# Kernel tuning notes

Hardware: AMD Instinct MI355X
Metric: run time of the kernel (lower is better)

Reference implementation:

```python
import jax, jax.numpy as jnp
import numpy as np

DIM = 512  # word_hidden_size * 2


def _linear_params(key, din, dout, scale=0.05):
    kw, kb = jax.random.split(key)
    W = jax.random.normal(kw, (din, dout), dtype=jnp.float32) * scale
    b = jax.random.normal(kb, (dout,), dtype=jnp.float32) * scale
    return W, b


def setup_inputs() -> dict:
    key = jax.random.key(0)
    ks = jax.random.split(key, 16)
    S_c, S_q, B = 256, 32, 32
    inp = {
        'context_output': jax.random.normal(ks[0], (S_c, B, DIM), dtype=jnp.float32),
        'question_output': jax.random.normal(ks[1], (S_q, B, DIM), dtype=jnp.float32),
        'question_hidden_state': jax.random.normal(ks[2], (B, DIM), dtype=jnp.float32),
        'image_output': jax.random.normal(ks[3], (S_c, B, DIM), dtype=jnp.float32),
    }
    names = ['fc1', 'fc2', 'dm', 'rm', 'qm', 'rr', 'rg', 'qg']
    for i, n in enumerate(names):
        W, b = _linear_params(ks[4 + i], DIM, DIM)
        inp['W_' + n] = W
        inp['b_' + n] = b
    W_ms, b_ms = _linear_params(ks[12], DIM, 1)
    inp['W_ms'] = W_ms
    inp['b_ms'] = b_ms
    return inp


def reference(context_output, question_output, question_hidden_state, image_output,
              W_fc1, b_fc1, W_fc2, b_fc2, W_dm, b_dm, W_rm, b_rm, W_qm, b_qm,
              W_rr, b_rr, W_rg, b_rg, W_qg, b_qg, W_ms, b_ms):
    # ctx: [B, S, D] = fc1(context) + fc2(image) after seq-first -> batch-first permute
    ctx = (jnp.einsum('sbd,de->bse', context_output, W_fc1) + b_fc1
           + jnp.einsum('sbd,de->bse', image_output, W_fc2) + b_fc2)
    # hoist loop-invariant linear_dm(ctx): same math, computed once
    ctx_dm = jnp.einsum('bsd,de->bse', ctx, W_dm) + b_dm  # [B, S, D]

    B = ctx.shape[0]
    r0 = jnp.zeros((B, DIM), dtype=ctx.dtype)

    def step(r, q_t):  # r: [B, D], q_t: [B, D]
        rm = r @ W_rm + b_rm          # [B, D]
        qm = q_t @ W_qm + b_qm        # [B, D]
        m = jnp.tanh(ctx_dm + rm[:, None, :] + qm[:, None, :])  # [B, S, D]
        logits = jnp.einsum('bsd,do->bso', m, W_ms)[..., 0] + b_ms[0]  # [B, S]
        s = jax.nn.softmax(logits, axis=1)                     # [B, S]
        r_new = jnp.einsum('bs,bsd->bd', s, ctx) + jnp.tanh(r @ W_rr + b_rr)
        return r_new, None

    r, _ = jax.lax.scan(step, r0, question_output)  # scan over question tokens

    g = (r @ W_rg + b_rg) + (question_hidden_state @ W_qg + b_qg)  # [B, D]
    return g
```

## Files before the change

### kernel.cpp

```cpp
#include <hip/hip_runtime.h>
#include <hip/hip_bf16.h>

#define DIMD 512
#define NB   32
#define NS   256
#define NT   32
#define SA_STR  66
#define SCT_STR 258
#define SR_STR  132

typedef __bf16 bf16x8 __attribute__((ext_vector_type(8)));
typedef float  f32x4  __attribute__((ext_vector_type(4)));

__device__ __forceinline__ float tanh_fast(float x) {
    float e = __expf(2.f * x);
    return 1.f - 2.f / (e + 1.f);
}

__device__ __forceinline__ void gl_lds16(const __bf16* g, __bf16* l) {
    __builtin_amdgcn_global_load_lds((const __attribute__((address_space(1))) void*)g,
                                     (__attribute__((address_space(3))) void*)l, 16, 0, 0);
}


__global__ void k_prep(const float* __restrict__ ctxin, const float* __restrict__ img,
                       const float* __restrict__ qin,
                       __bf16* __restrict__ acat, __bf16* __restrict__ qp) {
    int row = blockIdx.x;
    if (row < 8192) {
        int b = row >> 8, s = row & 255;
        const float* c  = ctxin + ((size_t)s * NB + b) * DIMD;
        const float* im = img   + ((size_t)s * NB + b) * DIMD;
        __bf16* o = acat + (size_t)row * 1024;
        for (int d = threadIdx.x; d < DIMD; d += 256) {
            o[d]       = (__bf16)c[d];
            o[512 + d] = (__bf16)im[d];
        }
    } else {
        int idx = (row - 8192) * 256 + threadIdx.x;
        qp[idx] = (__bf16)qin[idx];
    }
}

__global__ void k_transpose_w6(const float* __restrict__ s0, const float* __restrict__ s1,
                               const float* __restrict__ s2, const float* __restrict__ s3,
                               const float* __restrict__ s4_, const float* __restrict__ s5,
                               __bf16* __restrict__ d01, __bf16* __restrict__ d2,
                               __bf16* __restrict__ d3, __bf16* __restrict__ d4,
                               __bf16* __restrict__ d5) {
    __shared__ float tile[32][33];
    int z = blockIdx.z;
    const float* src = (z == 0) ? s0 : (z == 1) ? s1 : (z == 2) ? s2
                     : (z == 3) ? s3 : (z == 4) ? s4_ : s5;
    __bf16* dst; int stride, off;
    if (z < 2) { dst = d01; stride = 1024; off = z * 512; }
    else {
        dst = (z == 2) ? d2 : (z == 3) ? d3 : (z == 4) ? d4 : d5;
        stride = 512; off = 0;
    }
    int c0 = blockIdx.x * 32, r0 = blockIdx.y * 32;
    int x = threadIdx.x, y = threadIdx.y;
#pragma unroll
    for (int k = 0; k < 32; k += 8)
        tile[y + k][x] = src[(size_t)(r0 + y + k) * DIMD + c0 + x];
    __syncthreads();
#pragma unroll
    for (int k = 0; k < 32; k += 8)
        dst[(size_t)(c0 + y + k) * stride + off + r0 + x] = (__bf16)tile[x][y + k];
}

__global__ void k_post_t(const __bf16* __restrict__ ctxb, __bf16* __restrict__ ctxT,
                         const float* __restrict__ Wrg, const float* __restrict__ Wqg,
                         __bf16* __restrict__ wrgT, __bf16* __restrict__ wqgT) {
    int z = blockIdx.z;
    int x = threadIdx.x, y = threadIdx.y;
    if (z < 32) {
        if (blockIdx.y >= 8) return;
        __shared__ __bf16 tile[32][33];
        int c0 = blockIdx.x * 32, s0 = blockIdx.y * 32;
        const __bf16* S = ctxb + (size_t)z * NS * DIMD;
        __bf16* D = ctxT + (size_t)z * DIMD * NS;
#pragma unroll
        for (int k = 0; k < 32; k += 8)
            tile[y + k][x] = S[(size_t)(s0 + y + k) * DIMD + c0 + x];
        __syncthreads();
#pragma unroll
        for (int k = 0; k < 32; k += 8)
            D[(size_t)(c0 + y + k) * NS + s0 + x] = tile[x][y + k];
    } else {
        __shared__ float tf[32][33];
        const float* src = (z == 32) ? Wrg : Wqg;
        __bf16* dst = (z == 32) ? wrgT : wqgT;
        int c0 = blockIdx.x * 32, r0 = blockIdx.y * 32;
#pragma unroll
        for (int k = 0; k < 32; k += 8)
            tf[y + k][x] = src[(size_t)(r0 + y + k) * DIMD + c0 + x];
        __syncthreads();
#pragma unroll
        for (int k = 0; k < 32; k += 8)
            dst[(size_t)(c0 + y + k) * DIMD + r0 + x] = (__bf16)tf[x][y + k];
    }
}

__global__ void k_gemm64(const __bf16* __restrict__ A, const __bf16* __restrict__ BT,
                         const float* __restrict__ bias1, const float* __restrict__ bias2,
                         void* __restrict__ out, int M, int N, int K, int out_f32) {
    __shared__ __bf16 As[64 * 64];
    __shared__ __bf16 Bs[64 * 64];
    int tid = threadIdx.x, wave = tid >> 6, lane = tid & 63;
    int wm = wave >> 1, wn = wave & 1;
    int m0 = blockIdx.x * 64, n0 = blockIdx.y * 64;
    int lr = lane & 15, lq = lane >> 4;

    f32x4 acc[2][2];
#pragma unroll
    for (int i = 0; i < 2; i++)
#pragma unroll
        for (int j = 0; j < 2; j++) acc[i][j] = (f32x4){0.f, 0.f, 0.f, 0.f};

    int g0 = (wave * 2 + 0) * 64 + lane;
    int g1 = (wave * 2 + 1) * 64 + lane;
    int r0_ = g0 >> 3, c0_ = g0 & 7;
    int r1_ = g1 >> 3, c1_ = g1 & 7;
    __bf16* la0 = As + (wave * 2 + 0) * 512;
    __bf16* la1 = As + (wave * 2 + 1) * 512;
    __bf16* lb0 = Bs + (wave * 2 + 0) * 512;
    __bf16* lb1 = Bs + (wave * 2 + 1) * 512;

    for (int kk = 0; kk < K; kk += 64) {
        gl_lds16(A  + (size_t)(m0 + r0_) * K + kk + c0_ * 8, la0);
        gl_lds16(A  + (size_t)(m0 + r1_) * K + kk + c1_ * 8, la1);
        gl_lds16(BT + (size_t)(n0 + r0_) * K + kk + c0_ * 8, lb0);
        gl_lds16(BT + (size_t)(n0 + r1_) * K + kk + c1_ * 8, lb1);
        __syncthreads();
#pragma unroll
        for (int k2 = 0; k2 < 64; k2 += 32) {
            bf16x8 af[2], bfv[2];
#pragma unroll
            for (int i = 0; i < 2; i++)
                af[i] = *(const bf16x8*)(As + (wm * 32 + i * 16 + lr) * 64 + k2 + lq * 8);
#pragma unroll
            for (int j = 0; j < 2; j++)
                bfv[j] = *(const bf16x8*)(Bs + (wn * 32 + j * 16 + lr) * 64 + k2 + lq * 8);
#pragma unroll
            for (int i = 0; i < 2; i++)
#pragma unroll
                for (int j = 0; j < 2; j++)
                    acc[i][j] = __builtin_amdgcn_mfma_f32_16x16x32_bf16(af[i], bfv[j], acc[i][j], 0, 0, 0);
        }
        __syncthreads();
    }

#pragma unroll
    for (int i = 0; i < 2; i++)
#pragma unroll
        for (int j = 0; j < 2; j++) {
            int col = n0 + wn * 32 + j * 16 + lr;
            float bs = bias1[col] + (bias2 ? bias2[col] : 0.f);
#pragma unroll
            for (int r = 0; r < 4; r++) {
                int row = m0 + wm * 32 + i * 16 + lq * 4 + r;
                float v = acc[i][j][r] + bs;
                if (out_f32) ((float*)out)[(size_t)row * N + col] = v;
                else         ((__bf16*)out)[(size_t)row * N + col] = (__bf16)v;
            }
        }
}


__device__ __forceinline__ void bflag(unsigned* fb, int j, unsigned tgt) {
    __syncthreads();
    if (threadIdx.x == 0) {
        __atomic_signal_fence(__ATOMIC_SEQ_CST);
        __builtin_amdgcn_s_waitcnt(0x0F70);
        __atomic_signal_fence(__ATOMIC_SEQ_CST);
        __hip_atomic_store(fb + j * 16, tgt, __ATOMIC_RELAXED, __HIP_MEMORY_SCOPE_AGENT);
    }
    if (threadIdx.x < 8) {
        while (__hip_atomic_load(fb + threadIdx.x * 16, __ATOMIC_RELAXED,
                                 __HIP_MEMORY_SCOPE_AGENT) < tgt)
            __builtin_amdgcn_s_sleep(1);
    }
    __syncthreads();
}

__global__ __launch_bounds__(512, 2) void k_scan(
    const __bf16* __restrict__ ctxdm,
    const __bf16* __restrict__ ctxT,
    const __bf16* __restrict__ wrmT,
    const __bf16* __restrict__ wrrT,
    const float* __restrict__ qmf,
    const float* __restrict__ wms, const float* __restrict__ brm,
    const float* __restrict__ brr,
    float* partials,
    float* rpub,
    unsigned* flags,
    float* __restrict__ rbuf) {
    int bid = blockIdx.x;
    int b = bid >> 3, j = bid & 7;
    int tid = threadIdx.x, wave = tid >> 6, lane = tid & 63;
    int g = lane >> 3, i = lane & 7;

    __shared__ __bf16 sA[256 * SA_STR];
    __shared__ __bf16 sCT[64 * SCT_STR];
    __shared__ float  sQ[NT * 64];
    __shared__ float  spart[NS];
    __shared__ float  sp[NS];
    __shared__ float  sq[512];
    __shared__ float  s4[4];
    __shared__ float  sps[8 * 68];
    __shared__ float  srm[64], sh[64];
    __shared__ float  sr4[4 * SR_STR];
    __shared__ float  smv[512];

    unsigned* fb = flags + b * 8 * 16;

    for (int c = tid; c < 2048; c += 512) {
        int row = c >> 3, c8 = c & 7;
        *(bf16x8*)(sA + row * SA_STR + c8 * 8) =
            *(const bf16x8*)(ctxdm + ((size_t)(b * NS + row)) * DIMD + j * 64 + c8 * 8);
    }
    for (int c = tid; c < 2048; c += 512) {
        int col = c >> 5, s8 = c & 31;
        *(bf16x8*)(sCT + col * SCT_STR + s8 * 8) =
            *(const bf16x8*)(ctxT + ((size_t)(b * DIMD) + j * 64 + col) * NS + s8 * 8);
    }
    for (int c = tid; c < NT * 64; c += 512) {
        int tt = c >> 6, e = c & 63;
        sQ[c] = qmf[((size_t)tt * NB + b) * DIMD + j * 64 + e];
    }
    int m = tid >> 8, cl = (tid >> 2) & 63, q = tid & 3;
    const __bf16* wp = (m ? wrrT : wrmT) + ((size_t)(j * 64 + cl)) * DIMD + q * 128;
    bf16x8 wreg[16];
#pragma unroll
    for (int u = 0; u < 16; u++) wreg[u] = *(const bf16x8*)(wp + u * 8);

    float wm[8];
#pragma unroll
    for (int u = 0; u < 8; u++) wm[u] = wms[j * 64 + i * 8 + u];
    if (tid < 64) {
        srm[tid] = brm[j * 64 + tid];
        sh[tid]  = tanh_fast(brr[j * 64 + tid]);
    }
    __syncthreads();

    unsigned ph = 1;
    for (int t = 0; t < NT; t++) {
        float rq[8];
#pragma unroll
        for (int u = 0; u < 8; u++) rq[u] = srm[i * 8 + u] + sQ[t * 64 + i * 8 + u];
#pragma unroll
        for (int k = 0; k < 4; k++) {
            int s = wave * 32 + k * 8 + g;
            bf16x8 cv = *(const bf16x8*)(sA + s * SA_STR + i * 8);
            float a = 0.f;
#pragma unroll
            for (int u = 0; u < 8; u++)
                a += tanh_fast((float)cv[u] + rq[u]) * wm[u];
            a += __shfl_xor(a, 1); a += __shfl_xor(a, 2); a += __shfl_xor(a, 4);
            if (i == 0) spart[s] = a;
        }
        __syncthreads();
        if (tid < NS)
            __hip_atomic_store(&partials[(b * 8 + j) * NS + tid], spart[tid],
                               __ATOMIC_RELAXED, __HIP_MEMORY_SCOPE_AGENT);
        bflag(fb, j, ph); ph++;

        {
            int s = tid >> 1, jh = (tid & 1) * 4;
            float a = 0.f;
#pragma unroll
            for (int u = 0; u < 4; u++)
                a += __hip_atomic_load(&partials[(b * 8 + jh + u) * NS + s],
                                       __ATOMIC_RELAXED, __HIP_MEMORY_SCOPE_AGENT);
            sq[tid] = a;
        }
        __syncthreads();
        float ev = 0.f;
        if (tid < NS) { ev = __expf(sq[2 * tid] + sq[2 * tid + 1]); sp[tid] = ev; }
#pragma unroll
        for (int off = 32; off; off >>= 1) ev += __shfl_xor(ev, off);
        if (tid < NS && lane == 0) s4[wave] = ev;
        __syncthreads();
        float inv = 1.f / (s4[0] + s4[1] + s4[2] + s4[3]);
        {
            const __bf16* cp = sCT + lane * SCT_STR + wave * 32;
            const float* pp = sp + wave * 32;
            float a = 0.f;
#pragma unroll
            for (int k = 0; k < 32; k += 8) {
                bf16x8 v = *(const bf16x8*)(cp + k);
#pragma unroll
                for (int u = 0; u < 8; u++) a = fmaf(pp[k + u], (float)v[u], a);
            }
            sps[wave * 68 + lane] = a;
        }
        __syncthreads();
        if (tid < 64) {
            float a = 0.f;
#pragma unroll
            for (int w2 = 0; w2 < 8; w2++) a += sps[w2 * 68 + tid];
            float rv = a * inv + sh[tid];
            if (t == NT - 1) rbuf[b * DIMD + j * 64 + tid] = rv;
            else
                __hip_atomic_store(&rpub[b * DIMD + j * 64 + tid], rv,
                                   __ATOMIC_RELAXED, __HIP_MEMORY_SCOPE_AGENT);
        }
        if (t == NT - 1) break;
        bflag(fb, j, ph); ph++;

        sr4[(tid >> 7) * SR_STR + (tid & 127)] =
            __hip_atomic_load(&rpub[b * DIMD + tid], __ATOMIC_RELAXED, __HIP_MEMORY_SCOPE_AGENT);
        __syncthreads();
        {
            const float* sv = sr4 + q * SR_STR;
            float a0 = 0.f, a1 = 0.f;
#pragma unroll
            for (int u = 0; u < 16; u += 2) {
                bf16x8 w0 = wreg[u], w1 = wreg[u + 1];
#pragma unroll
                for (int e = 0; e < 8; e++) {
                    a0 = fmaf(sv[u * 8 + e],     (float)w0[e], a0);
                    a1 = fmaf(sv[u * 8 + 8 + e], (float)w1[e], a1);
                }
            }
            smv[tid] = a0 + a1;
        }
        __syncthreads();
        if (tid < 128) {
            int m2 = tid >> 6, cl3 = tid & 63;
            float a = smv[m2 * 256 + cl3 * 4] + smv[m2 * 256 + cl3 * 4 + 1]
                    + smv[m2 * 256 + cl3 * 4 + 2] + smv[m2 * 256 + cl3 * 4 + 3];
            int col = j * 64 + cl3;
            if (m2 == 0) srm[cl3] = a + brm[col];
            else         sh[cl3]  = tanh_fast(a + brr[col]);
        }
        __syncthreads();
    }
}

__global__ void k_final2(const float* __restrict__ r, const float* __restrict__ qh,
                         const __bf16* __restrict__ wrgT, const __bf16* __restrict__ wqgT,
                         const float* __restrict__ brg, const float* __restrict__ bqg,
                         float* __restrict__ out) {
    int clx = threadIdx.x & 7, b = threadIdx.x >> 3;
    int col = blockIdx.x * 8 + clx;
    const __bf16* w1 = wrgT + (size_t)col * DIMD;
    const __bf16* w2 = wqgT + (size_t)col * DIMD;
    const float* rp = r + (size_t)b * DIMD;
    const float* qp = qh + (size_t)b * DIMD;
    float acc = brg[col] + bqg[col];
#pragma unroll 4
    for (int d = 0; d < DIMD; d += 8) {
        bf16x8 a = *(const bf16x8*)(w1 + d);
        bf16x8 c = *(const bf16x8*)(w2 + d);
#pragma unroll
        for (int u = 0; u < 8; u++)
            acc += rp[d + u] * (float)a[u] + qp[d + u] * (float)c[u];
    }
    out[b * DIMD + col] = acc;
}


extern "C" void kernel_launch(void* const* d_in, const int* in_sizes, int n_in,
                              void* d_out, int out_size, void* d_ws, size_t ws_size,
                              hipStream_t stream) {
    const float* ctx_in = (const float*)d_in[0];
    const float* q_in   = (const float*)d_in[1];
    const float* qh     = (const float*)d_in[2];
    const float* img    = (const float*)d_in[3];
    const float* W_fc1  = (const float*)d_in[4];
    const float* b_fc1  = (const float*)d_in[5];
    const float* W_fc2  = (const float*)d_in[6];
    const float* b_fc2  = (const float*)d_in[7];
    const float* W_dm   = (const float*)d_in[8];
    const float* b_dm   = (const float*)d_in[9];
    const float* W_rm   = (const float*)d_in[10];
    const float* b_rm   = (const float*)d_in[11];
    const float* W_qm   = (const float*)d_in[12];
    const float* b_qm   = (const float*)d_in[13];
    const float* W_rr   = (const float*)d_in[14];
    const float* b_rr   = (const float*)d_in[15];
    const float* W_rg   = (const float*)d_in[16];
    const float* b_rg   = (const float*)d_in[17];
    const float* W_qg   = (const float*)d_in[18];
    const float* b_qg   = (const float*)d_in[19];
    const float* W_ms   = (const float*)d_in[20];

    char* w = (char*)d_ws;
    __bf16* acat  = (__bf16*)w;  w += (size_t)8192 * 1024 * 2;
    __bf16* qp    = (__bf16*)w;  w += (size_t)1024 * 512 * 2;
    __bf16* wcatT = (__bf16*)w;  w += (size_t)512 * 1024 * 2;
    __bf16* wdmT  = (__bf16*)w;  w += (size_t)512 * 512 * 2;
    __bf16* wqmT  = (__bf16*)w;  w += (size_t)512 * 512 * 2;
    __bf16* wrmT2 = (__bf16*)w;  w += (size_t)512 * 512 * 2;
    __bf16* wrrT2 = (__bf16*)w;  w += (size_t)512 * 512 * 2;
    __bf16* ctxb  = (__bf16*)w;  w += (size_t)8192 * 512 * 2;
    __bf16* ctxdm = (__bf16*)w;  w += (size_t)8192 * 512 * 2;
    char* x = (char*)acat;
    __bf16*   ctxT  = (__bf16*)x;    x += (size_t)NB * DIMD * NS * 2;
    float*    qmf   = (float*)x;     x += (size_t)1024 * 512 * 4;
    __bf16*   wrgT  = (__bf16*)x;    x += (size_t)512 * 512 * 2;
    __bf16*   wqgT  = (__bf16*)x;    x += (size_t)512 * 512 * 2;
    float*    rpub  = (float*)x;     x += (size_t)NB * DIMD * 4;
    float*    parts = (float*)x;     x += (size_t)NB * 8 * NS * 4;
    float*    rbuf  = (float*)x;     x += (size_t)NB * DIMD * 4;
    unsigned* flags = (unsigned*)x;  x += (size_t)256 * 16 * 4;

    k_prep<<<10240, 256, 0, stream>>>(ctx_in, img, q_in, acat, qp);
    k_transpose_w6<<<dim3(16, 16, 6), dim3(32, 8), 0, stream>>>(
        W_fc1, W_fc2, W_dm, W_qm, W_rm, W_rr, wcatT, wdmT, wqmT, wrmT2, wrrT2);

    k_gemm64<<<dim3(128, 8), 256, 0, stream>>>(acat, wcatT, b_fc1, b_fc2, ctxb, 8192, 512, 1024, 0);
    k_post_t<<<dim3(16, 16, 34), dim3(32, 8), 0, stream>>>(ctxb, ctxT, W_rg, W_qg, wrgT, wqgT);
    k_gemm64<<<dim3(128, 8), 256, 0, stream>>>(ctxb, wdmT, b_dm, nullptr, ctxdm, 8192, 512, 512, 0);
    k_gemm64<<<dim3(16, 8), 256, 0, stream>>>(qp, wqmT, b_qm, nullptr, qmf, 1024, 512, 512, 1);

    hipMemsetAsync(flags, 0, (size_t)256 * 16 * 4, stream);

    k_scan<<<256, 512, 0, stream>>>(ctxdm, ctxT, wrmT2, wrrT2, qmf, W_ms,
                                    b_rm, b_rr, parts, rpub, flags, rbuf);

    k_final2<<<64, 256, 0, stream>>>(rbuf, qh, wrgT, wqgT, b_rg, b_qg, (float*)d_out);
}
```

Measured before the change: 501.3 us.

## Fold fc and dm projections into one wide GEMM with precomputed combined weights

Precomputes the product of the concatenated fc1/fc2 weights with W_dm, plus a matching folded bias, so ctx and ctx_dm come out of a single 8192x1024x1024 GEMM reading the concatenated input. This replaces the two dependent GEMMs, removing the serial dependency on the intermediate ctx and one kernel launch. The scan kernel now reads ctx_dm from the upper half of the combined buffer, and its block-to-(batch, slice) mapping is also reordered. The cost is a small extra weight GEMM, and ctx_dm picks up slightly different bf16 rounding because it is computed from the raw inputs rather than from rounded ctx.

```diff
diff --git a/kernel.cpp b/kernel.cpp
--- a/kernel.cpp
+++ b/kernel.cpp
@@ -24,8 +24,10 @@
 
 
 __global__ void k_prep(const float* __restrict__ ctxin, const float* __restrict__ img,
-                       const float* __restrict__ qin,
-                       __bf16* __restrict__ acat, __bf16* __restrict__ qp) {
+                       const float* __restrict__ qin, const float* __restrict__ Wfc1,
+                       const float* __restrict__ Wfc2,
+                       __bf16* __restrict__ acat, __bf16* __restrict__ qp,
+                       __bf16* __restrict__ wcat_nt) {
     int row = blockIdx.x;
     if (row < 8192) {
         int b = row >> 8, s = row & 255;
@@ -36,9 +38,12 @@
             o[d]       = (__bf16)c[d];
             o[512 + d] = (__bf16)im[d];
         }
-    } else {
+    } else if (row < 10240) {
         int idx = (row - 8192) * 256 + threadIdx.x;
         qp[idx] = (__bf16)qin[idx];
+    } else {
+        int idx = (row - 10240) * 256 + threadIdx.x;
+        wcat_nt[idx] = (__bf16)(idx < 262144 ? Wfc1[idx] : Wfc2[idx - 262144]);
     }
 }
 
@@ -69,7 +74,19 @@
         dst[(size_t)(c0 + y + k) * stride + off + r0 + x] = (__bf16)tile[x][y + k];
 }
 
-__global__ void k_post_t(const __bf16* __restrict__ ctxb, __bf16* __restrict__ ctxT,
+__global__ void k_bias(const float* __restrict__ bfc1, const float* __restrict__ bfc2,
+                       const float* __restrict__ Wdm, const float* __restrict__ bdm,
+                       float* __restrict__ bias_big) {
+    int o = blockIdx.x * 256 + threadIdx.x;
+    if (o < 512) { bias_big[o] = bfc1[o] + bfc2[o]; return; }
+    int od = o - 512;
+    float acc = bdm[od];
+    for (int d = 0; d < 512; d++)
+        acc += (bfc1[d] + bfc2[d]) * Wdm[(size_t)d * 512 + od];
+    bias_big[o] = acc;
+}
+
+__global__ void k_post_t(const __bf16* __restrict__ ctxbig, __bf16* __restrict__ ctxT,
                          const float* __restrict__ Wrg, const float* __restrict__ Wqg,
                          __bf16* __restrict__ wrgT, __bf16* __restrict__ wqgT) {
     int z = blockIdx.z;
@@ -78,11 +95,11 @@
         if (blockIdx.y >= 8) return;
         __shared__ __bf16 tile[32][33];
         int c0 = blockIdx.x * 32, s0 = blockIdx.y * 32;
-        const __bf16* S = ctxb + (size_t)z * NS * DIMD;
+        const __bf16* S = ctxbig + (size_t)z * NS * 1024;
         __bf16* D = ctxT + (size_t)z * DIMD * NS;
 #pragma unroll
         for (int k = 0; k < 32; k += 8)
-            tile[y + k][x] = S[(size_t)(s0 + y + k) * DIMD + c0 + x];
+            tile[y + k][x] = S[(size_t)(s0 + y + k) * 1024 + c0 + x];
         __syncthreads();
 #pragma unroll
         for (int k = 0; k < 32; k += 8)
@@ -156,7 +173,7 @@
 #pragma unroll
         for (int j = 0; j < 2; j++) {
             int col = n0 + wn * 32 + j * 16 + lr;
-            float bs = bias1[col] + (bias2 ? bias2[col] : 0.f);
+            float bs = (bias1 ? bias1[col] : 0.f) + (bias2 ? bias2[col] : 0.f);
 #pragma unroll
             for (int r = 0; r < 4; r++) {
                 int row = m0 + wm * 32 + i * 16 + lq * 4 + r;
@@ -185,7 +202,7 @@
 }
 
 __global__ __launch_bounds__(512, 2) void k_scan(
-    const __bf16* __restrict__ ctxdm,
+    const __bf16* __restrict__ ctxbig,
     const __bf16* __restrict__ ctxT,
     const __bf16* __restrict__ wrmT,
     const __bf16* __restrict__ wrrT,
@@ -197,7 +214,7 @@
     unsigned* flags,
     float* __restrict__ rbuf) {
     int bid = blockIdx.x;
-    int b = bid >> 3, j = bid & 7;
+    int b = bid & 31, j = bid >> 5;
     int tid = threadIdx.x, wave = tid >> 6, lane = tid & 63;
     int g = lane >> 3, i = lane & 7;
 
@@ -218,7 +235,7 @@
     for (int c = tid; c < 2048; c += 512) {
         int row = c >> 3, c8 = c & 7;
         *(bf16x8*)(sA + row * SA_STR + c8 * 8) =
-            *(const bf16x8*)(ctxdm + ((size_t)(b * NS + row)) * DIMD + j * 64 + c8 * 8);
+            *(const bf16x8*)(ctxbig + ((size_t)(b * NS + row)) * 1024 + 512 + j * 64 + c8 * 8);
     }
     for (int c = tid; c < 2048; c += 512) {
         int col = c >> 5, s8 = c & 31;
@@ -388,15 +405,16 @@
     const float* W_ms   = (const float*)d_in[20];
 
     char* w = (char*)d_ws;
-    __bf16* acat  = (__bf16*)w;  w += (size_t)8192 * 1024 * 2;
-    __bf16* qp    = (__bf16*)w;  w += (size_t)1024 * 512 * 2;
-    __bf16* wcatT = (__bf16*)w;  w += (size_t)512 * 1024 * 2;
-    __bf16* wdmT  = (__bf16*)w;  w += (size_t)512 * 512 * 2;
-    __bf16* wqmT  = (__bf16*)w;  w += (size_t)512 * 512 * 2;
-    __bf16* wrmT2 = (__bf16*)w;  w += (size_t)512 * 512 * 2;
-    __bf16* wrrT2 = (__bf16*)w;  w += (size_t)512 * 512 * 2;
-    __bf16* ctxb  = (__bf16*)w;  w += (size_t)8192 * 512 * 2;
-    __bf16* ctxdm = (__bf16*)w;  w += (size_t)8192 * 512 * 2;
+    __bf16* acat   = (__bf16*)w;  w += (size_t)8192 * 1024 * 2;
+    __bf16* qp     = (__bf16*)w;  w += (size_t)1024 * 512 * 2;
+    __bf16* btc    = (__bf16*)w;  w += (size_t)1024 * 1024 * 2;
+    __bf16* wdmT   = (__bf16*)w;  w += (size_t)512 * 512 * 2;
+    __bf16* wqmT   = (__bf16*)w;  w += (size_t)512 * 512 * 2;
+    __bf16* wrmT2  = (__bf16*)w;  w += (size_t)512 * 512 * 2;
+    __bf16* wrrT2  = (__bf16*)w;  w += (size_t)512 * 512 * 2;
+    float*  biasb  = (float*)w;   w += (size_t)1024 * 4;
+    __bf16* ctxbig = (__bf16*)w;  w += (size_t)8192 * 1024 * 2;
+    __bf16* wcat_nt = ctxbig;
     char* x = (char*)acat;
     __bf16*   ctxT  = (__bf16*)x;    x += (size_t)NB * DIMD * NS * 2;
     float*    qmf   = (float*)x;     x += (size_t)1024 * 512 * 4;
@@ -407,18 +425,20 @@
     float*    rbuf  = (float*)x;     x += (size_t)NB * DIMD * 4;
     unsigned* flags = (unsigned*)x;  x += (size_t)256 * 16 * 4;
 
-    k_prep<<<10240, 256, 0, stream>>>(ctx_in, img, q_in, acat, qp);
+    k_prep<<<12288, 256, 0, stream>>>(ctx_in, img, q_in, W_fc1, W_fc2, acat, qp, wcat_nt);
     k_transpose_w6<<<dim3(16, 16, 6), dim3(32, 8), 0, stream>>>(
-        W_fc1, W_fc2, W_dm, W_qm, W_rm, W_rr, wcatT, wdmT, wqmT, wrmT2, wrrT2);
-
-    k_gemm64<<<dim3(128, 8), 256, 0, stream>>>(acat, wcatT, b_fc1, b_fc2, ctxb, 8192, 512, 1024, 0);
-    k_post_t<<<dim3(16, 16, 34), dim3(32, 8), 0, stream>>>(ctxb, ctxT, W_rg, W_qg, wrgT, wqgT);
-    k_gemm64<<<dim3(128, 8), 256, 0, stream>>>(ctxb, wdmT, b_dm, nullptr, ctxdm, 8192, 512, 512, 0);
+        W_fc1, W_fc2, W_dm, W_qm, W_rm, W_rr, btc, wdmT, wqmT, wrmT2, wrrT2);
+    k_bias<<<4, 256, 0, stream>>>(b_fc1, b_fc2, W_dm, b_dm, biasb);
+    k_gemm64<<<dim3(8, 16), 256, 0, stream>>>(wdmT, wcat_nt, nullptr, nullptr,
+                                              btc + (size_t)512 * 1024, 512, 1024, 512, 0);
+    k_gemm64<<<dim3(128, 16), 256, 0, stream>>>(acat, btc, biasb, nullptr,
+                                                ctxbig, 8192, 1024, 1024, 0);
+    k_post_t<<<dim3(16, 16, 34), dim3(32, 8), 0, stream>>>(ctxbig, ctxT, W_rg, W_qg, wrgT, wqgT);
     k_gemm64<<<dim3(16, 8), 256, 0, stream>>>(qp, wqmT, b_qm, nullptr, qmf, 1024, 512, 512, 1);
 
     hipMemsetAsync(flags, 0, (size_t)256 * 16 * 4, stream);
 
-    k_scan<<<256, 512, 0, stream>>>(ctxdm, ctxT, wrmT2, wrrT2, qmf, W_ms,
+    k_scan<<<256, 512, 0, stream>>>(ctxbig, ctxT, wrmT2, wrrT2, qmf, W_ms,
                                     b_rm, b_rr, parts, rpub, flags, rbuf);
 
     k_final2<<<64, 256, 0, stream>>>(rbuf, qh, wrgT, wqgT, b_rg, b_qg, (float*)d_out);
```

New measurement: 525.1 us. 1.05x slower.

## Replace flag barriers with tagged 64-bit publish/poll and fuse prep kernels

Applied to the files above, without the earlier changes.

The per-step flag barriers in the recurrent scan are replaced by packing each published float with a step tag in one 64-bit atomic word. Consumers spin on exactly the values they need instead of waiting on a group-wide flag barrier. This removes two barrier rounds per step and the flag memset. Block indexing is remapped so that the eight blocks sharing a batch row are spaced 32 apart. The input-cast and weight-transpose kernels are merged into one launch. The tradeoff is doubled traffic for the published data, and correctness depends on stale tags in reused workspace never matching the current step.

```diff
diff --git a/kernel.cpp b/kernel.cpp
--- a/kernel.cpp
+++ b/kernel.cpp
@@ -11,6 +11,7 @@
 
 typedef __bf16 bf16x8 __attribute__((ext_vector_type(8)));
 typedef float  f32x4  __attribute__((ext_vector_type(4)));
+typedef unsigned long long u64;
 
 __device__ __forceinline__ float tanh_fast(float x) {
     float e = __expf(2.f * x);
@@ -22,10 +23,28 @@
                                      (__attribute__((address_space(3))) void*)l, 16, 0, 0);
 }
 
-
-__global__ void k_prep(const float* __restrict__ ctxin, const float* __restrict__ img,
-                       const float* __restrict__ qin,
-                       __bf16* __restrict__ acat, __bf16* __restrict__ qp) {
+__device__ __forceinline__ void pub64(u64* p, float v, unsigned tag) {
+    u64 pk = ((u64)__float_as_uint(v) << 32) | (u64)tag;
+    __hip_atomic_store(p, pk, __ATOMIC_RELAXED, __HIP_MEMORY_SCOPE_AGENT);
+}
+__device__ __forceinline__ float poll64(const u64* p, unsigned tag) {
+    u64 v = __hip_atomic_load(p, __ATOMIC_RELAXED, __HIP_MEMORY_SCOPE_AGENT);
+    while ((unsigned)v != tag) {
+        __builtin_amdgcn_s_sleep(1);
+        v = __hip_atomic_load(p, __ATOMIC_RELAXED, __HIP_MEMORY_SCOPE_AGENT);
+    }
+    return __uint_as_float((unsigned)(v >> 32));
+}
+
+__global__ void k_prep_all(const float* __restrict__ ctxin, const float* __restrict__ img,
+                           const float* __restrict__ qin,
+                           const float* __restrict__ Wfc1, const float* __restrict__ Wfc2,
+                           const float* __restrict__ Wdm, const float* __restrict__ Wqm,
+                           const float* __restrict__ Wrm, const float* __restrict__ Wrr,
+                           __bf16* __restrict__ acat, __bf16* __restrict__ qp,
+                           __bf16* __restrict__ wcatT, __bf16* __restrict__ wdmT,
+                           __bf16* __restrict__ wqmT, __bf16* __restrict__ wrmT,
+                           __bf16* __restrict__ wrrT) {
     int row = blockIdx.x;
     if (row < 8192) {
         int b = row >> 8, s = row & 255;
@@ -36,37 +55,32 @@
             o[d]       = (__bf16)c[d];
             o[512 + d] = (__bf16)im[d];
         }
-    } else {
+    } else if (row < 10240) {
         int idx = (row - 8192) * 256 + threadIdx.x;
         qp[idx] = (__bf16)qin[idx];
-    }
-}
-
-__global__ void k_transpose_w6(const float* __restrict__ s0, const float* __restrict__ s1,
-                               const float* __restrict__ s2, const float* __restrict__ s3,
-                               const float* __restrict__ s4_, const float* __restrict__ s5,
-                               __bf16* __restrict__ d01, __bf16* __restrict__ d2,
-                               __bf16* __restrict__ d3, __bf16* __restrict__ d4,
-                               __bf16* __restrict__ d5) {
-    __shared__ float tile[32][33];
-    int z = blockIdx.z;
-    const float* src = (z == 0) ? s0 : (z == 1) ? s1 : (z == 2) ? s2
-                     : (z == 3) ? s3 : (z == 4) ? s4_ : s5;
-    __bf16* dst; int stride, off;
-    if (z < 2) { dst = d01; stride = 1024; off = z * 512; }
-    else {
-        dst = (z == 2) ? d2 : (z == 3) ? d3 : (z == 4) ? d4 : d5;
-        stride = 512; off = 0;
-    }
-    int c0 = blockIdx.x * 32, r0 = blockIdx.y * 32;
-    int x = threadIdx.x, y = threadIdx.y;
-#pragma unroll
-    for (int k = 0; k < 32; k += 8)
-        tile[y + k][x] = src[(size_t)(r0 + y + k) * DIMD + c0 + x];
-    __syncthreads();
-#pragma unroll
-    for (int k = 0; k < 32; k += 8)
-        dst[(size_t)(c0 + y + k) * stride + off + r0 + x] = (__bf16)tile[x][y + k];
+    } else {
+        __shared__ float tile[32][33];
+        int zz = (row - 10240) >> 8;
+        int idx = (row - 10240) & 255;
+        int bx = idx & 15, by = idx >> 4;
+        int x = threadIdx.x & 31, y = threadIdx.x >> 5;
+        const float* src = (zz == 0) ? Wfc1 : (zz == 1) ? Wfc2 : (zz == 2) ? Wdm
+                         : (zz == 3) ? Wqm : (zz == 4) ? Wrm : Wrr;
+        __bf16* dst; int stride, off;
+        if (zz < 2) { dst = wcatT; stride = 1024; off = zz * 512; }
+        else {
+            dst = (zz == 2) ? wdmT : (zz == 3) ? wqmT : (zz == 4) ? wrmT : wrrT;
+            stride = 512; off = 0;
+        }
+        int c0 = bx * 32, r0 = by * 32;
+#pragma unroll
+        for (int k = 0; k < 32; k += 8)
+            tile[y + k][x] = src[(size_t)(r0 + y + k) * DIMD + c0 + x];
+        __syncthreads();
+#pragma unroll
+        for (int k = 0; k < 32; k += 8)
+            dst[(size_t)(c0 + y + k) * stride + off + r0 + x] = (__bf16)tile[x][y + k];
+    }
 }
 
 __global__ void k_post_t(const __bf16* __restrict__ ctxb, __bf16* __restrict__ ctxT,
@@ -156,7 +170,7 @@
 #pragma unroll
         for (int j = 0; j < 2; j++) {
             int col = n0 + wn * 32 + j * 16 + lr;
-            float bs = bias1[col] + (bias2 ? bias2[col] : 0.f);
+            float bs = (bias1 ? bias1[col] : 0.f) + (bias2 ? bias2[col] : 0.f);
 #pragma unroll
             for (int r = 0; r < 4; r++) {
                 int row = m0 + wm * 32 + i * 16 + lq * 4 + r;
@@ -165,23 +179,6 @@
                 else         ((__bf16*)out)[(size_t)row * N + col] = (__bf16)v;
             }
         }
-}
-
-
-__device__ __forceinline__ void bflag(unsigned* fb, int j, unsigned tgt) {
-    __syncthreads();
-    if (threadIdx.x == 0) {
-        __atomic_signal_fence(__ATOMIC_SEQ_CST);
-        __builtin_amdgcn_s_waitcnt(0x0F70);
-        __atomic_signal_fence(__ATOMIC_SEQ_CST);
-        __hip_atomic_store(fb + j * 16, tgt, __ATOMIC_RELAXED, __HIP_MEMORY_SCOPE_AGENT);
-    }
-    if (threadIdx.x < 8) {
-        while (__hip_atomic_load(fb + threadIdx.x * 16, __ATOMIC_RELAXED,
-                                 __HIP_MEMORY_SCOPE_AGENT) < tgt)
-            __builtin_amdgcn_s_sleep(1);
-    }
-    __syncthreads();
 }
 
 __global__ __launch_bounds__(512, 2) void k_scan(
@@ -192,12 +189,11 @@
     const float* __restrict__ qmf,
     const float* __restrict__ wms, const float* __restrict__ brm,
     const float* __restrict__ brr,
-    float* partials,
-    float* rpub,
-    unsigned* flags,
+    u64* parts,
+    u64* rpub,
     float* __restrict__ rbuf) {
     int bid = blockIdx.x;
-    int b = bid >> 3, j = bid & 7;
+    int b = bid & 31, j = bid >> 5;
     int tid = threadIdx.x, wave = tid >> 6, lane = tid & 63;
     int g = lane >> 3, i = lane & 7;
 
@@ -205,7 +201,6 @@
     __shared__ __bf16 sCT[64 * SCT_STR];
     __shared__ float  sQ[NT * 64];
     __shared__ float  spart[NS];
-    __shared__ float  sp[NS];
     __shared__ float  sq[512];
     __shared__ float  s4[4];
     __shared__ float  sps[8 * 68];
@@ -213,8 +208,6 @@
     __shared__ float  sr4[4 * SR_STR];
     __shared__ float  smv[512];
 
-    unsigned* fb = flags + b * 8 * 16;
-
     for (int c = tid; c < 2048; c += 512) {
         int row = c >> 3, c8 = c & 7;
         *(bf16x8*)(sA + row * SA_STR + c8 * 8) =
@@ -244,8 +237,8 @@
     }
     __syncthreads();
 
-    unsigned ph = 1;
     for (int t = 0; t < NT; t++) {
+        unsigned tag = (unsigned)(t + 1);
         float rq[8];
 #pragma unroll
         for (int u = 0; u < 8; u++) rq[u] = srm[i * 8 + u] + sQ[t * 64 + i * 8 + u];
@@ -262,22 +255,20 @@
         }
         __syncthreads();
         if (tid < NS)
-            __hip_atomic_store(&partials[(b * 8 + j) * NS + tid], spart[tid],
-                               __ATOMIC_RELAXED, __HIP_MEMORY_SCOPE_AGENT);
-        bflag(fb, j, ph); ph++;
+            pub64(&parts[(b * 8 + j) * NS + tid], spart[tid], tag);
 
         {
             int s = tid >> 1, jh = (tid & 1) * 4;
             float a = 0.f;
 #pragma unroll
             for (int u = 0; u < 4; u++)
-                a += __hip_atomic_load(&partials[(b * 8 + jh + u) * NS + s],
-                                       __ATOMIC_RELAXED, __HIP_MEMORY_SCOPE_AGENT);
+                a += poll64(&parts[(b * 8 + jh + u) * NS + s], tag);
             sq[tid] = a;
         }
         __syncthreads();
         float ev = 0.f;
-        if (tid < NS) { ev = __expf(sq[2 * tid] + sq[2 * tid + 1]); sp[tid] = ev; }
+        if (tid < NS) { ev = __expf(sq[2 * tid] + sq[2 * tid + 1]); sq[tid] = ev; }
+        else sq[tid] = 0.f;
 #pragma unroll
         for (int off = 32; off; off >>= 1) ev += __shfl_xor(ev, off);
         if (tid < NS && lane == 0) s4[wave] = ev;
@@ -285,7 +276,7 @@
         float inv = 1.f / (s4[0] + s4[1] + s4[2] + s4[3]);
         {
             const __bf16* cp = sCT + lane * SCT_STR + wave * 32;
-            const float* pp = sp + wave * 32;
+            const float* pp = sq + wave * 32;
             float a = 0.f;
 #pragma unroll
             for (int k = 0; k < 32; k += 8) {
@@ -302,15 +293,11 @@
             for (int w2 = 0; w2 < 8; w2++) a += sps[w2 * 68 + tid];
             float rv = a * inv + sh[tid];
             if (t == NT - 1) rbuf[b * DIMD + j * 64 + tid] = rv;
-            else
-                __hip_atomic_store(&rpub[b * DIMD + j * 64 + tid], rv,
-                                   __ATOMIC_RELAXED, __HIP_MEMORY_SCOPE_AGENT);
+            else             pub64(&rpub[b * DIMD + j * 64 + tid], rv, tag);
         }
         if (t == NT - 1) break;
-        bflag(fb, j, ph); ph++;
-
-        sr4[(tid >> 7) * SR_STR + (tid & 127)] =
-            __hip_atomic_load(&rpub[b * DIMD + tid], __ATOMIC_RELAXED, __HIP_MEMORY_SCOPE_AGENT);
+
+        sr4[(tid >> 7) * SR_STR + (tid & 127)] = poll64(&rpub[b * DIMD + tid], tag);
         __syncthreads();
         {
             const float* sv = sr4 + q * SR_STR;
@@ -393,33 +380,29 @@
     __bf16* wcatT = (__bf16*)w;  w += (size_t)512 * 1024 * 2;
     __bf16* wdmT  = (__bf16*)w;  w += (size_t)512 * 512 * 2;
     __bf16* wqmT  = (__bf16*)w;  w += (size_t)512 * 512 * 2;
-    __bf16* wrmT2 = (__bf16*)w;  w += (size_t)512 * 512 * 2;
-    __bf16* wrrT2 = (__bf16*)w;  w += (size_t)512 * 512 * 2;
+    __bf16* wrmT  = (__bf16*)w;  w += (size_t)512 * 512 * 2;
+    __bf16* wrrT  = (__bf16*)w;  w += (size_t)512 * 512 * 2;
     __bf16* ctxb  = (__bf16*)w;  w += (size_t)8192 * 512 * 2;
     __bf16* ctxdm = (__bf16*)w;  w += (size_t)8192 * 512 * 2;
     char* x = (char*)acat;
-    __bf16*   ctxT  = (__bf16*)x;    x += (size_t)NB * DIMD * NS * 2;
-    float*    qmf   = (float*)x;     x += (size_t)1024 * 512 * 4;
-    __bf16*   wrgT  = (__bf16*)x;    x += (size_t)512 * 512 * 2;
-    __bf16*   wqgT  = (__bf16*)x;    x += (size_t)512 * 512 * 2;
-    float*    rpub  = (float*)x;     x += (size_t)NB * DIMD * 4;
-    float*    parts = (float*)x;     x += (size_t)NB * 8 * NS * 4;
-    float*    rbuf  = (float*)x;     x += (size_t)NB * DIMD * 4;
-    unsigned* flags = (unsigned*)x;  x += (size_t)256 * 16 * 4;
-
-    k_prep<<<10240, 256, 0, stream>>>(ctx_in, img, q_in, acat, qp);
-    k_transpose_w6<<<dim3(16, 16, 6), dim3(32, 8), 0, stream>>>(
-        W_fc1, W_fc2, W_dm, W_qm, W_rm, W_rr, wcatT, wdmT, wqmT, wrmT2, wrrT2);
-
+    __bf16* ctxT  = (__bf16*)x;  x += (size_t)NB * DIMD * NS * 2;
+    float*  qmf   = (float*)x;   x += (size_t)1024 * 512 * 4;
+    __bf16* wrgT  = (__bf16*)x;  x += (size_t)512 * 512 * 2;
+    __bf16* wqgT  = (__bf16*)x;  x += (size_t)512 * 512 * 2;
+    u64*    rpub  = (u64*)x;     x += (size_t)NB * DIMD * 8;
+    u64*    parts = (u64*)x;     x += (size_t)NB * 8 * NS * 8;
+    float*  rbuf  = (float*)x;   x += (size_t)NB * DIMD * 4;
+
+    k_prep_all<<<11776, 256, 0, stream>>>(ctx_in, img, q_in, W_fc1, W_fc2, W_dm,
+                                          W_qm, W_rm, W_rr, acat, qp,
+                                          wcatT, wdmT, wqmT, wrmT, wrrT);
     k_gemm64<<<dim3(128, 8), 256, 0, stream>>>(acat, wcatT, b_fc1, b_fc2, ctxb, 8192, 512, 1024, 0);
     k_post_t<<<dim3(16, 16, 34), dim3(32, 8), 0, stream>>>(ctxb, ctxT, W_rg, W_qg, wrgT, wqgT);
     k_gemm64<<<dim3(128, 8), 256, 0, stream>>>(ctxb, wdmT, b_dm, nullptr, ctxdm, 8192, 512, 512, 0);
     k_gemm64<<<dim3(16, 8), 256, 0, stream>>>(qp, wqmT, b_qm, nullptr, qmf, 1024, 512, 512, 1);
 
-    hipMemsetAsync(flags, 0, (size_t)256 * 16 * 4, stream);
-
-    k_scan<<<256, 512, 0, stream>>>(ctxdm, ctxT, wrmT2, wrrT2, qmf, W_ms,
-                                    b_rm, b_rr, parts, rpub, flags, rbuf);
+    k_scan<<<256, 512, 0, stream>>>(ctxdm, ctxT, wrmT, wrrT, qmf, W_ms,
+                                    b_rm, b_rr, parts, rpub, rbuf);
 
     k_final2<<<64, 256, 0, stream>>>(rbuf, qh, wrgT, wqgT, b_rg, b_qg, (float*)d_out);
 }
```

After: 467.5 us. 6.7% less time.
